# Kernel tuning notes

Hardware: AMD Instinct MI355X
Metric: run time of the kernel (lower is better)

Reference implementation:

```python
import jax, jax.numpy as jnp
import numpy as np

B, N, D = 64, 5000, 128
EPS = 1e-5

def setup_inputs() -> dict:
    key = jax.random.key(0)
    ks = jax.random.split(key, 10)
    s = 1.0 / np.sqrt(D)
    s2 = 1.0 / np.sqrt(2 * D)
    return {
        "batch_size": B,
        "num_customers": N,
        "solution_neighbours": jax.random.randint(ks[0], (B, N, 2), 0, N + 1),
        "embeddings": jax.random.normal(ks[1], (B, N + 1, D), dtype=jnp.float32),
        "w_left": jax.random.uniform(ks[2], (D, D), jnp.float32, -s, s),
        "w_right": jax.random.uniform(ks[3], (D, D), jnp.float32, -s, s),
        "w_comb": jax.random.uniform(ks[4], (D, 2 * D), jnp.float32, -s2, s2),
        "b_comb": jax.random.uniform(ks[5], (D,), jnp.float32, -s2, s2),
        "w_ff": jax.random.uniform(ks[6], (D, D), jnp.float32, -s, s),
        "b_ff": jax.random.uniform(ks[7], (D,), jnp.float32, -s, s),
        "norm_w": jnp.ones((D,), jnp.float32),
        "norm_b": jnp.zeros((D,), jnp.float32),
    }

def _gather(emb, idx):
    # emb: (B, N+1, D), idx: (B, N) -> (B, N, D)
    d = emb.shape[-1]
    return jnp.take_along_axis(emb, jnp.broadcast_to(idx[:, :, None], idx.shape + (d,)), axis=1)

def reference(batch_size, num_customers, solution_neighbours, embeddings,
              w_left, w_right, w_comb, b_comb, w_ff, b_ff, norm_w, norm_b):
    left = _gather(embeddings, solution_neighbours[:, :, 0])
    right = _gather(embeddings, solution_neighbours[:, :, 1])
    # per-edge linear projections (directed graph: separate weights)
    info = left @ w_left.T + right @ w_right.T        # (B, N, D)
    cust = embeddings[:, 1:]                           # (B, N, D)
    combined = jnp.concatenate([cust, info], axis=2)   # (B, N, 2D)
    h = jax.nn.relu(combined @ w_comb.T + b_comb)
    h = h @ w_ff.T + b_ff
    # residual + InstanceNorm1d over the customer axis (per batch, per channel)
    added = cust + h
    mean = jnp.mean(added, axis=1, keepdims=True)
    var = jnp.mean(jnp.square(added - mean), axis=1, keepdims=True)  # biased var
    normed = (added - mean) * jax.lax.rsqrt(var + EPS) * norm_w + norm_b
    return jnp.concatenate([embeddings[:, :1], normed], axis=1)
```

## Files before the change

kernel.cpp:

```cpp
#include <hip/hip_runtime.h>

typedef unsigned short u16;
typedef __attribute__((ext_vector_type(8))) short bf16x8;
typedef __attribute__((ext_vector_type(4))) float f32x4;

#define BB 64
#define NN 5000
#define DD 128
#define EROW 640128
#define CROW 640000

__device__ __forceinline__ u16 f2bf(float f){
  unsigned u = __builtin_bit_cast(unsigned, f);
  u += 0x7fffu + ((u >> 16) & 1u);
  return (u16)(u >> 16);
}
__device__ __forceinline__ float bf2f(u16 h){
  unsigned u = ((unsigned)h) << 16;
  return __builtin_bit_cast(float, u);
}

__global__ __launch_bounds__(256) void k0_prep(
    const float* __restrict__ wl, const float* __restrict__ wr,
    const float* __restrict__ wcmb, const float* __restrict__ wff,
    const float* __restrict__ emb, float* __restrict__ out,
    u16* __restrict__ wbf, float* __restrict__ sums, float* __restrict__ sumsq)
{
  int t = blockIdx.x * 256 + threadIdx.x;
  if      (t < 16384) wbf[t] = f2bf(wl[t]);
  else if (t < 32768) wbf[t] = f2bf(wr[t - 16384]);
  else if (t < 65536) wbf[t] = f2bf(wcmb[t - 32768]);
  else                wbf[t] = f2bf(wff[t - 65536]);
  if (t < 8192){
    sums[t] = 0.f; sumsq[t] = 0.f;
    int b = t >> 7, d = t & 127;
    out[(size_t)b * EROW + d] = emb[(size_t)b * EROW + d];
  }
}

__global__ __launch_bounds__(256, 2)
void k1_main(const int2* __restrict__ sol, const float* __restrict__ emb,
             const u16* __restrict__ wbf, const float* __restrict__ b_comb,
             const float* __restrict__ b_ff, float* __restrict__ out,
             float* __restrict__ sums, float* __restrict__ sumsq)
{
  const int tid  = threadIdx.x;
  const int lane = tid & 63;
  const int wave = tid >> 6;
  const int q    = lane >> 4;
  const int c    = lane & 15;
  const int tile = blockIdx.x;
  const int b    = blockIdx.y;
  const int rbase = tile * 64;
  const int RC = min(64, NN - rbase);

  __shared__ u16 P0[64][136];
  __shared__ u16 P1[64][136];
  __shared__ u16 P2[64][136];
  __shared__ int sIL[64], sIR[64];

  if (tid < 64){
    int r = rbase + tid; r = min(r, NN - 1);
    int2 p = sol[(size_t)b * NN + r];
    sIL[tid] = p.x; sIR[tid] = p.y;
  }
  __syncthreads();

  {
    const int i = tid >> 2, sub = tid & 3;
    const float* embB = emb + (size_t)b * EROW;
    if (i < RC){
      const float4* vC = (const float4*)(embB + (size_t)(rbase + i + 1) * DD) + sub * 8;
      const float4* vL = (const float4*)(embB + (size_t)sIL[i] * DD) + sub * 8;
      const float4* vR = (const float4*)(embB + (size_t)sIR[i] * DD) + sub * 8;
      #pragma unroll
      for (int j = 0; j < 8; ++j){
        float4 a = vL[j], bb = vR[j], cc = vC[j];
        int col = sub * 32 + j * 4;
        ushort4 ua = {f2bf(a.x),  f2bf(a.y),  f2bf(a.z),  f2bf(a.w)};
        ushort4 ub = {f2bf(bb.x), f2bf(bb.y), f2bf(bb.z), f2bf(bb.w)};
        ushort4 uc = {f2bf(cc.x), f2bf(cc.y), f2bf(cc.z), f2bf(cc.w)};
        *(ushort4*)&P0[i][col] = ua;
        *(ushort4*)&P1[i][col] = ub;
        *(ushort4*)&P2[i][col] = uc;
      }
    } else {
      ushort4 z = {0,0,0,0};
      #pragma unroll
      for (int j = 0; j < 8; ++j){
        int col = sub * 32 + j * 4;
        *(ushort4*)&P0[i][col] = z;
        *(ushort4*)&P1[i][col] = z;
        *(ushort4*)&P2[i][col] = z;
      }
    }
  }
  __syncthreads();

  const int n0 = wave * 32 + c;
  const int n1 = n0 + 16;

  const u16* wl = wbf;
  const u16* wr = wbf + 16384;
  const u16* wc = wbf + 32768;
  const u16* wf = wbf + 65536;

  const f32x4 fz = {0.f, 0.f, 0.f, 0.f};
  f32x4 acc[4][2];

  #pragma unroll
  for (int mt = 0; mt < 4; ++mt){ acc[mt][0] = fz; acc[mt][1] = fz; }
  #pragma unroll
  for (int ks = 0; ks < 8; ++ks){
    const u16* W = (ks < 4) ? wl : wr;
    const int kk = (ks & 3) * 32 + q * 8;
    bf16x8 b0 = *(const bf16x8*)(W + n0 * 128 + kk);
    bf16x8 b1 = *(const bf16x8*)(W + n1 * 128 + kk);
    #pragma unroll
    for (int mt = 0; mt < 4; ++mt){
      bf16x8 a = *(const bf16x8*)&((ks < 4) ? P0 : P1)[mt * 16 + c][kk];
      acc[mt][0] = __builtin_amdgcn_mfma_f32_16x16x32_bf16(a, b0, acc[mt][0], 0, 0, 0);
      acc[mt][1] = __builtin_amdgcn_mfma_f32_16x16x32_bf16(a, b1, acc[mt][1], 0, 0, 0);
    }
  }
  __syncthreads();
  #pragma unroll
  for (int mt = 0; mt < 4; ++mt){
    #pragma unroll
    for (int r = 0; r < 4; ++r){
      int m = mt * 16 + q * 4 + r;
      P0[m][n0] = f2bf(acc[mt][0][r]);
      P0[m][n1] = f2bf(acc[mt][1][r]);
    }
  }
  __syncthreads();

  #pragma unroll
  for (int mt = 0; mt < 4; ++mt){ acc[mt][0] = fz; acc[mt][1] = fz; }
  #pragma unroll
  for (int ks = 0; ks < 8; ++ks){
    const int kk = (ks & 3) * 32 + q * 8;
    const int kg = ks * 32 + q * 8;
    bf16x8 b0 = *(const bf16x8*)(wc + n0 * 256 + kg);
    bf16x8 b1 = *(const bf16x8*)(wc + n1 * 256 + kg);
    #pragma unroll
    for (int mt = 0; mt < 4; ++mt){
      bf16x8 a = *(const bf16x8*)&((ks < 4) ? P2 : P0)[mt * 16 + c][kk];
      acc[mt][0] = __builtin_amdgcn_mfma_f32_16x16x32_bf16(a, b0, acc[mt][0], 0, 0, 0);
      acc[mt][1] = __builtin_amdgcn_mfma_f32_16x16x32_bf16(a, b1, acc[mt][1], 0, 0, 0);
    }
  }
  __syncthreads();
  {
    float bc0 = b_comb[n0], bc1 = b_comb[n1];
    #pragma unroll
    for (int mt = 0; mt < 4; ++mt){
      #pragma unroll
      for (int r = 0; r < 4; ++r){
        int m = mt * 16 + q * 4 + r;
        P1[m][n0] = f2bf(fmaxf(acc[mt][0][r] + bc0, 0.f));
        P1[m][n1] = f2bf(fmaxf(acc[mt][1][r] + bc1, 0.f));
      }
    }
  }
  __syncthreads();

  #pragma unroll
  for (int mt = 0; mt < 4; ++mt){ acc[mt][0] = fz; acc[mt][1] = fz; }
  #pragma unroll
  for (int ks = 0; ks < 4; ++ks){
    const int kk = ks * 32 + q * 8;
    bf16x8 b0 = *(const bf16x8*)(wf + n0 * 128 + kk);
    bf16x8 b1 = *(const bf16x8*)(wf + n1 * 128 + kk);
    #pragma unroll
    for (int mt = 0; mt < 4; ++mt){
      bf16x8 a = *(const bf16x8*)&P1[mt * 16 + c][kk];
      acc[mt][0] = __builtin_amdgcn_mfma_f32_16x16x32_bf16(a, b0, acc[mt][0], 0, 0, 0);
      acc[mt][1] = __builtin_amdgcn_mfma_f32_16x16x32_bf16(a, b1, acc[mt][1], 0, 0, 0);
    }
  }

  float bf0 = b_ff[n0], bf1 = b_ff[n1];
  float sv0 = 0.f, sq0 = 0.f, sv1 = 0.f, sq1 = 0.f;
  float* outB = out + (size_t)b * EROW;
  #pragma unroll
  for (int mt = 0; mt < 4; ++mt){
    #pragma unroll
    for (int r = 0; r < 4; ++r){
      int m = mt * 16 + q * 4 + r;
      if (m < RC){
        float v0 = acc[mt][0][r] + bf0 + bf2f(P2[m][n0]);
        float v1 = acc[mt][1][r] + bf1 + bf2f(P2[m][n1]);
        size_t ro = (size_t)(rbase + m + 1) * DD;
        outB[ro + n0] = v0;
        outB[ro + n1] = v1;
        sv0 += v0; sq0 += v0 * v0;
        sv1 += v1; sq1 += v1 * v1;
      }
    }
  }
  sv0 += __shfl_xor(sv0, 16); sv0 += __shfl_xor(sv0, 32);
  sq0 += __shfl_xor(sq0, 16); sq0 += __shfl_xor(sq0, 32);
  sv1 += __shfl_xor(sv1, 16); sv1 += __shfl_xor(sv1, 32);
  sq1 += __shfl_xor(sq1, 16); sq1 += __shfl_xor(sq1, 32);
  if (q == 0){
    atomicAdd(&sums [b * DD + n0], sv0);
    atomicAdd(&sumsq[b * DD + n0], sq0);
    atomicAdd(&sums [b * DD + n1], sv1);
    atomicAdd(&sumsq[b * DD + n1], sq1);
  }
}

__global__ __launch_bounds__(256) void k1b_stats(
    const float* __restrict__ sums, const float* __restrict__ sumsq,
    const float* __restrict__ nw, const float* __restrict__ nb,
    float* __restrict__ scale, float* __restrict__ shift)
{
  int t = blockIdx.x * 256 + threadIdx.x;
  int d = t & 127;
  float mean = sums[t] * (1.f / NN);
  float var  = sumsq[t] * (1.f / NN) - mean * mean;
  float inv  = rsqrtf(var + 1e-5f);
  float sc = inv * nw[d];
  scale[t] = sc;
  shift[t] = nb[d] - mean * sc;
}

__global__ __launch_bounds__(256) void k2_norm(
    float* __restrict__ out, const float* __restrict__ scale, const float* __restrict__ shift)
{
  size_t t = (size_t)blockIdx.x * 256 + threadIdx.x;
  size_t e = t * 8;
  int b = (int)(e / CROW);
  int rem = (int)(e - (size_t)b * CROW);
  int d = rem & 127;
  const float4 s0 = *(const float4*)&scale[b * DD + d];
  const float4 s1 = *(const float4*)&scale[b * DD + d + 4];
  const float4 h0 = *(const float4*)&shift[b * DD + d];
  const float4 h1 = *(const float4*)&shift[b * DD + d + 4];
  float4* p = (float4*)(out + (size_t)b * EROW + DD + rem);
  float4 v0 = p[0], v1 = p[1];
  v0.x = v0.x * s0.x + h0.x; v0.y = v0.y * s0.y + h0.y;
  v0.z = v0.z * s0.z + h0.z; v0.w = v0.w * s0.w + h0.w;
  v1.x = v1.x * s1.x + h1.x; v1.y = v1.y * s1.y + h1.y;
  v1.z = v1.z * s1.z + h1.z; v1.w = v1.w * s1.w + h1.w;
  p[0] = v0; p[1] = v1;
}

extern "C" void kernel_launch(void* const* d_in, const int* in_sizes, int n_in,
                              void* d_out, int out_size, void* d_ws, size_t ws_size,
                              hipStream_t stream)
{
  const int2*  sol  = (const int2*) d_in[2];
  const float* emb  = (const float*)d_in[3];
  const float* wl   = (const float*)d_in[4];
  const float* wr   = (const float*)d_in[5];
  const float* wcmb = (const float*)d_in[6];
  const float* bcmb = (const float*)d_in[7];
  const float* wff  = (const float*)d_in[8];
  const float* bff  = (const float*)d_in[9];
  const float* nw   = (const float*)d_in[10];
  const float* nb   = (const float*)d_in[11];
  float* out = (float*)d_out;

  u16*   wbf   = (u16*)d_ws;
  float* sums  = (float*)((char*)d_ws + 163840);
  float* sumsq = (float*)((char*)d_ws + 196608);
  float* scale = (float*)((char*)d_ws + 229376);
  float* shift = (float*)((char*)d_ws + 262144);

  k0_prep <<<320, 256, 0, stream>>>(wl, wr, wcmb, wff, emb, out, wbf, sums, sumsq);
  k1_main <<<dim3(79, 64), 256, 0, stream>>>(sol, emb, wbf, bcmb, bff, out, sums, sumsq);
  k1b_stats<<<32, 256, 0, stream>>>(sums, sumsq, nw, nb, scale, shift);
  k2_norm <<<20000, 256, 0, stream>>>(out, scale, shift);
}
```

Baseline: 504.5 us.

## Stage pre-norm activations as bf16 in workspace and trim LDS for higher occupancy

```diff
diff --git a/kernel.cpp b/kernel.cpp
--- a/kernel.cpp
+++ b/kernel.cpp
@@ -38,11 +38,12 @@
   }
 }
 
-__global__ __launch_bounds__(256, 2)
+template<bool BF>
+__global__ __launch_bounds__(256, 4)
 void k1_main(const int2* __restrict__ sol, const float* __restrict__ emb,
              const u16* __restrict__ wbf, const float* __restrict__ b_comb,
              const float* __restrict__ b_ff, float* __restrict__ out,
-             float* __restrict__ sums, float* __restrict__ sumsq)
+             u16* __restrict__ abuf, float* __restrict__ sums, float* __restrict__ sumsq)
 {
   const int tid  = threadIdx.x;
   const int lane = tid & 63;
@@ -54,9 +55,8 @@
   const int rbase = tile * 64;
   const int RC = min(64, NN - rbase);
 
-  __shared__ u16 P0[64][136];
-  __shared__ u16 P1[64][136];
-  __shared__ u16 P2[64][136];
+  __shared__ u16 A[64][136];
+  __shared__ u16 Bb[64][136];
   __shared__ int sIL[64], sIR[64];
 
   if (tid < 64){
@@ -66,33 +66,21 @@
   }
   __syncthreads();
 
+  const float* embB = emb + (size_t)b * EROW;
+  const int gi = tid >> 2, gsub = tid & 3;
+
   {
-    const int i = tid >> 2, sub = tid & 3;
-    const float* embB = emb + (size_t)b * EROW;
-    if (i < RC){
-      const float4* vC = (const float4*)(embB + (size_t)(rbase + i + 1) * DD) + sub * 8;
-      const float4* vL = (const float4*)(embB + (size_t)sIL[i] * DD) + sub * 8;
-      const float4* vR = (const float4*)(embB + (size_t)sIR[i] * DD) + sub * 8;
-      #pragma unroll
-      for (int j = 0; j < 8; ++j){
-        float4 a = vL[j], bb = vR[j], cc = vC[j];
-        int col = sub * 32 + j * 4;
-        ushort4 ua = {f2bf(a.x),  f2bf(a.y),  f2bf(a.z),  f2bf(a.w)};
-        ushort4 ub = {f2bf(bb.x), f2bf(bb.y), f2bf(bb.z), f2bf(bb.w)};
-        ushort4 uc = {f2bf(cc.x), f2bf(cc.y), f2bf(cc.z), f2bf(cc.w)};
-        *(ushort4*)&P0[i][col] = ua;
-        *(ushort4*)&P1[i][col] = ub;
-        *(ushort4*)&P2[i][col] = uc;
-      }
-    } else {
-      ushort4 z = {0,0,0,0};
-      #pragma unroll
-      for (int j = 0; j < 8; ++j){
-        int col = sub * 32 + j * 4;
-        *(ushort4*)&P0[i][col] = z;
-        *(ushort4*)&P1[i][col] = z;
-        *(ushort4*)&P2[i][col] = z;
-      }
+    int il = sIL[gi], ir = sIR[gi];
+    const float4* vL = (const float4*)(embB + (size_t)il * DD) + gsub * 8;
+    const float4* vR = (const float4*)(embB + (size_t)ir * DD) + gsub * 8;
+    #pragma unroll
+    for (int j = 0; j < 8; ++j){
+      float4 a = vL[j], bb = vR[j];
+      int col = gsub * 32 + j * 4;
+      ushort4 ua = {f2bf(a.x),  f2bf(a.y),  f2bf(a.z),  f2bf(a.w)};
+      ushort4 ub = {f2bf(bb.x), f2bf(bb.y), f2bf(bb.z), f2bf(bb.w)};
+      *(ushort4*)&A[gi][col]  = ua;
+      *(ushort4*)&Bb[gi][col] = ub;
     }
   }
   __syncthreads();
@@ -118,19 +106,31 @@
     bf16x8 b1 = *(const bf16x8*)(W + n1 * 128 + kk);
     #pragma unroll
     for (int mt = 0; mt < 4; ++mt){
-      bf16x8 a = *(const bf16x8*)&((ks < 4) ? P0 : P1)[mt * 16 + c][kk];
+      bf16x8 a = *(const bf16x8*)&((ks < 4) ? A : Bb)[mt * 16 + c][kk];
       acc[mt][0] = __builtin_amdgcn_mfma_f32_16x16x32_bf16(a, b0, acc[mt][0], 0, 0, 0);
       acc[mt][1] = __builtin_amdgcn_mfma_f32_16x16x32_bf16(a, b1, acc[mt][1], 0, 0, 0);
     }
   }
   __syncthreads();
+
   #pragma unroll
   for (int mt = 0; mt < 4; ++mt){
     #pragma unroll
     for (int r = 0; r < 4; ++r){
       int m = mt * 16 + q * 4 + r;
-      P0[m][n0] = f2bf(acc[mt][0][r]);
-      P0[m][n1] = f2bf(acc[mt][1][r]);
+      A[m][n0] = f2bf(acc[mt][0][r]);
+      A[m][n1] = f2bf(acc[mt][1][r]);
+    }
+  }
+  {
+    int crow = min(rbase + gi + 1, NN);
+    const float4* vC = (const float4*)(embB + (size_t)crow * DD) + gsub * 8;
+    #pragma unroll
+    for (int j = 0; j < 8; ++j){
+      float4 cc = vC[j];
+      int col = gsub * 32 + j * 4;
+      ushort4 uc = {f2bf(cc.x), f2bf(cc.y), f2bf(cc.z), f2bf(cc.w)};
+      *(ushort4*)&Bb[gi][col] = uc;
     }
   }
   __syncthreads();
@@ -145,7 +145,7 @@
     bf16x8 b1 = *(const bf16x8*)(wc + n1 * 256 + kg);
     #pragma unroll
     for (int mt = 0; mt < 4; ++mt){
-      bf16x8 a = *(const bf16x8*)&((ks < 4) ? P2 : P0)[mt * 16 + c][kk];
+      bf16x8 a = *(const bf16x8*)&((ks < 4) ? Bb : A)[mt * 16 + c][kk];
       acc[mt][0] = __builtin_amdgcn_mfma_f32_16x16x32_bf16(a, b0, acc[mt][0], 0, 0, 0);
       acc[mt][1] = __builtin_amdgcn_mfma_f32_16x16x32_bf16(a, b1, acc[mt][1], 0, 0, 0);
     }
@@ -158,8 +158,8 @@
       #pragma unroll
       for (int r = 0; r < 4; ++r){
         int m = mt * 16 + q * 4 + r;
-        P1[m][n0] = f2bf(fmaxf(acc[mt][0][r] + bc0, 0.f));
-        P1[m][n1] = f2bf(fmaxf(acc[mt][1][r] + bc1, 0.f));
+        A[m][n0] = f2bf(fmaxf(acc[mt][0][r] + bc0, 0.f));
+        A[m][n1] = f2bf(fmaxf(acc[mt][1][r] + bc1, 0.f));
       }
     }
   }
@@ -174,13 +174,13 @@
     bf16x8 b1 = *(const bf16x8*)(wf + n1 * 128 + kk);
     #pragma unroll
     for (int mt = 0; mt < 4; ++mt){
-      bf16x8 a = *(const bf16x8*)&P1[mt * 16 + c][kk];
+      bf16x8 a = *(const bf16x8*)&A[mt * 16 + c][kk];
       acc[mt][0] = __builtin_amdgcn_mfma_f32_16x16x32_bf16(a, b0, acc[mt][0], 0, 0, 0);
       acc[mt][1] = __builtin_amdgcn_mfma_f32_16x16x32_bf16(a, b1, acc[mt][1], 0, 0, 0);
     }
   }
 
-  float bf0 = b_ff[n0], bf1 = b_ff[n1];
+  const float bf0 = b_ff[n0], bf1 = b_ff[n1];
   float sv0 = 0.f, sq0 = 0.f, sv1 = 0.f, sq1 = 0.f;
   float* outB = out + (size_t)b * EROW;
   #pragma unroll
@@ -188,14 +188,17 @@
     #pragma unroll
     for (int r = 0; r < 4; ++r){
       int m = mt * 16 + q * 4 + r;
+      float v0 = acc[mt][0][r] + bf0 + bf2f(Bb[m][n0]);
+      float v1 = acc[mt][1][r] + bf1 + bf2f(Bb[m][n1]);
+      acc[mt][0][r] = v0; acc[mt][1][r] = v1;
       if (m < RC){
-        float v0 = acc[mt][0][r] + bf0 + bf2f(P2[m][n0]);
-        float v1 = acc[mt][1][r] + bf1 + bf2f(P2[m][n1]);
-        size_t ro = (size_t)(rbase + m + 1) * DD;
-        outB[ro + n0] = v0;
-        outB[ro + n1] = v1;
         sv0 += v0; sq0 += v0 * v0;
         sv1 += v1; sq1 += v1 * v1;
+        if (!BF){
+          size_t ro = (size_t)(rbase + m + 1) * DD;
+          outB[ro + n0] = v0;
+          outB[ro + n1] = v1;
+        }
       }
     }
   }
@@ -209,6 +212,27 @@
     atomicAdd(&sums [b * DD + n1], sv1);
     atomicAdd(&sumsq[b * DD + n1], sq1);
   }
+
+  if (BF){
+    __syncthreads();
+    #pragma unroll
+    for (int mt = 0; mt < 4; ++mt){
+      #pragma unroll
+      for (int r = 0; r < 4; ++r){
+        int m = mt * 16 + q * 4 + r;
+        A[m][n0] = f2bf(acc[mt][0][r]);
+        A[m][n1] = f2bf(acc[mt][1][r]);
+      }
+    }
+    __syncthreads();
+    const int row = tid >> 2, cb = tid & 3;
+    if (rbase + row < NN){
+      u16* dst = abuf + ((size_t)b * NN + rbase + row) * DD + cb * 32;
+      #pragma unroll
+      for (int j = 0; j < 4; ++j)
+        *(bf16x8*)(dst + j * 8) = *(const bf16x8*)&A[row][cb * 32 + j * 8];
+    }
+  }
 }
 
 __global__ __launch_bounds__(256) void k1b_stats(
@@ -226,19 +250,48 @@
   shift[t] = nb[d] - mean * sc;
 }
 
-__global__ __launch_bounds__(256) void k2_norm(
-    float* __restrict__ out, const float* __restrict__ scale, const float* __restrict__ shift)
-{
-  size_t t = (size_t)blockIdx.x * 256 + threadIdx.x;
-  size_t e = t * 8;
-  int b = (int)(e / CROW);
-  int rem = (int)(e - (size_t)b * CROW);
-  int d = rem & 127;
+__global__ __launch_bounds__(256) void k2_bf(
+    const u16* __restrict__ abuf, const float* __restrict__ scale,
+    const float* __restrict__ shift, float* __restrict__ out)
+{
+  const int b = blockIdx.y;
+  const int e = (blockIdx.x * 256 + threadIdx.x) * 8;
+  if (e >= CROW) return;
+  const int d = e & 127;
+  const uint4 raw = *(const uint4*)(abuf + (size_t)b * CROW + e);
   const float4 s0 = *(const float4*)&scale[b * DD + d];
   const float4 s1 = *(const float4*)&scale[b * DD + d + 4];
   const float4 h0 = *(const float4*)&shift[b * DD + d];
   const float4 h1 = *(const float4*)&shift[b * DD + d + 4];
-  float4* p = (float4*)(out + (size_t)b * EROW + DD + rem);
+  float4 v0, v1;
+  v0.x = __builtin_bit_cast(float, raw.x << 16);
+  v0.y = __builtin_bit_cast(float, raw.x & 0xffff0000u);
+  v0.z = __builtin_bit_cast(float, raw.y << 16);
+  v0.w = __builtin_bit_cast(float, raw.y & 0xffff0000u);
+  v1.x = __builtin_bit_cast(float, raw.z << 16);
+  v1.y = __builtin_bit_cast(float, raw.z & 0xffff0000u);
+  v1.z = __builtin_bit_cast(float, raw.w << 16);
+  v1.w = __builtin_bit_cast(float, raw.w & 0xffff0000u);
+  v0.x = v0.x * s0.x + h0.x; v0.y = v0.y * s0.y + h0.y;
+  v0.z = v0.z * s0.z + h0.z; v0.w = v0.w * s0.w + h0.w;
+  v1.x = v1.x * s1.x + h1.x; v1.y = v1.y * s1.y + h1.y;
+  v1.z = v1.z * s1.z + h1.z; v1.w = v1.w * s1.w + h1.w;
+  float4* p = (float4*)(out + (size_t)b * EROW + DD + e);
+  p[0] = v0; p[1] = v1;
+}
+
+__global__ __launch_bounds__(256) void k2_rmw(
+    float* __restrict__ out, const float* __restrict__ scale, const float* __restrict__ shift)
+{
+  const int b = blockIdx.y;
+  const int e = (blockIdx.x * 256 + threadIdx.x) * 8;
+  if (e >= CROW) return;
+  const int d = e & 127;
+  const float4 s0 = *(const float4*)&scale[b * DD + d];
+  const float4 s1 = *(const float4*)&scale[b * DD + d + 4];
+  const float4 h0 = *(const float4*)&shift[b * DD + d];
+  const float4 h1 = *(const float4*)&shift[b * DD + d + 4];
+  float4* p = (float4*)(out + (size_t)b * EROW + DD + e);
   float4 v0 = p[0], v1 = p[1];
   v0.x = v0.x * s0.x + h0.x; v0.y = v0.y * s0.y + h0.y;
   v0.z = v0.z * s0.z + h0.z; v0.w = v0.w * s0.w + h0.w;
@@ -268,9 +321,19 @@
   float* sumsq = (float*)((char*)d_ws + 196608);
   float* scale = (float*)((char*)d_ws + 229376);
   float* shift = (float*)((char*)d_ws + 262144);
+  u16*   abuf  = (u16*)((char*)d_ws + 294912);
+
+  const size_t need = 294912ull + (size_t)BB * NN * DD * 2;
+  const bool bfpath = (ws_size >= need);
 
   k0_prep <<<320, 256, 0, stream>>>(wl, wr, wcmb, wff, emb, out, wbf, sums, sumsq);
-  k1_main <<<dim3(79, 64), 256, 0, stream>>>(sol, emb, wbf, bcmb, bff, out, sums, sumsq);
-  k1b_stats<<<32, 256, 0, stream>>>(sums, sumsq, nw, nb, scale, shift);
-  k2_norm <<<20000, 256, 0, stream>>>(out, scale, shift);
-}
+  if (bfpath){
+    k1_main<true> <<<dim3(79, 64), 256, 0, stream>>>(sol, emb, wbf, bcmb, bff, out, abuf, sums, sumsq);
+    k1b_stats<<<32, 256, 0, stream>>>(sums, sumsq, nw, nb, scale, shift);
+    k2_bf  <<<dim3(313, 64), 256, 0, stream>>>(abuf, scale, shift, out);
+  } else {
+    k1_main<false><<<dim3(79, 64), 256, 0, stream>>>(sol, emb, wbf, bcmb, bff, out, abuf, sums, sumsq);
+    k1b_stats<<<32, 256, 0, stream>>>(sums, sumsq, nw, nb, scale, shift);
+    k2_rmw <<<dim3(313, 64), 256, 0, stream>>>(out, scale, shift);
+  }
+}
```

After: 483.9 us. 1.04x faster.
